# Optimization experiments

Measured on AMD Instinct MI355X. Metric: run time of the kernel, lower is better.

## Reference

```python
import jax, jax.numpy as jnp
import numpy as np

B, L, D_IN, D_MODEL, D_STATE, D_DISCR, KER = 2, 1024, 512, 1024, 16, 64, 4


def setup_inputs() -> dict:
    ks = jax.random.split(jax.random.key(0), 9)
    s = 0.02
    return {
        "seq": jax.random.normal(ks[0], (B, L, D_IN), jnp.float32),
        "W_in": jax.random.normal(ks[1], (2 * D_MODEL, D_IN), jnp.float32) * s,
        "W_out": jax.random.normal(ks[2], (D_IN, D_MODEL), jnp.float32) * s,
        "W_B": jax.random.normal(ks[3], (D_STATE, D_MODEL), jnp.float32) * s,
        "W_C": jax.random.normal(ks[4], (D_STATE, D_MODEL), jnp.float32) * s,
        "W_D1": jax.random.normal(ks[5], (D_DISCR, D_MODEL), jnp.float32) * s,
        "W_D2": jax.random.normal(ks[6], (D_MODEL, D_DISCR), jnp.float32) * s,
        "conv_w": jax.random.normal(ks[7], (D_MODEL, 1, KER), jnp.float32) * 0.1,
        "conv_b": jax.random.normal(ks[8], (D_MODEL,), jnp.float32) * 0.01,
        "A": jnp.tile(jnp.arange(1, D_STATE + 1, dtype=jnp.float32), (D_MODEL, 1)),
        "D": jnp.ones((D_MODEL,), jnp.float32),
    }


def _causal_depthwise_conv(x, w, b):
    # x: [B, L, D] -> torch Conv1d(groups=D, padding=KER-1) truncated to first L outputs
    x = jnp.swapaxes(x, 1, 2)  # [B, D, L]
    y = jax.lax.conv_general_dilated(
        x, w, window_strides=(1,), padding=[(KER - 1, 0)],
        dimension_numbers=("NCH", "OIH", "NCH"), feature_group_count=D_MODEL)
    y = y + b[None, :, None]
    return jnp.swapaxes(y, 1, 2)  # [B, L, D]


def _ssm(x, W_B, W_C, W_D1, W_D2, A, D):
    # x: [B, L, D]
    exp_negA = jnp.exp(-A)                                  # [D, S]
    Bm = jnp.einsum("bld,sd->bls", x, W_B)                  # [B, L, S]
    Cm = jnp.einsum("bld,sd->bls", x, W_C)                  # [B, L, S]
    delta = jax.nn.softplus(D + jnp.einsum("ble,de->bld", jnp.einsum("bld,ed->ble", x, W_D1), W_D2))  # [B, L, D]
    A_bar = exp_negA[None, None] * delta[..., None]         # [B, L, D, S]
    X = Bm[:, :, None, :] * delta[..., None] * x[..., None]  # [B, L, D, S]

    def comb(c1, c2):
        a1, x1 = c1
        a2, x2 = c2
        return a1 * a2, a2 * x1 + x2

    _, h = jax.lax.associative_scan(comb, (A_bar, X), axis=1)  # h: [B, L, D, S]
    y = jnp.einsum("blds,bls->bld", h, Cm)
    return y + D * x


def reference(seq, W_in, W_out, W_B, W_C, W_D1, W_D2, conv_w, conv_b, A, D):
    ab = jnp.einsum("bli,oi->blo", seq, W_in)   # [B, L, 2*D_MODEL]
    a, b = ab[..., :D_MODEL], ab[..., D_MODEL:]
    a = jax.nn.silu(_causal_depthwise_conv(a, conv_w, conv_b))
    a = _ssm(a, W_B, W_C, W_D1, W_D2, A, D)
    out = a * jax.nn.silu(b)
    return jnp.einsum("bld,od->blo", out, W_out)  # [B, L, D_IN]
```

## Files before the change

### kernel.cpp

```cpp
#include <hip/hip_runtime.h>
#include <hip/hip_bf16.h>

using bf16 = __hip_bfloat16;
typedef short short8 __attribute__((ext_vector_type(8)));
typedef float float4v __attribute__((ext_vector_type(4)));

#define B_   2
#define L_   1024
#define DIN  512
#define DM   1024
#define DS   16
#define DD   64
#define KER_ 4
#define NROW (B_*L_)

#define SD   8
#define SC   32
#define SLC  32
#define SDP  9

__device__ __forceinline__ float silu_f(float v){ return v / (1.f + expf(-v)); }

__device__ __forceinline__ short f2bf(float f) {
  union { float f; unsigned u; } v; v.f = f;
  return (short)((v.u + 0x7FFF + ((v.u >> 16) & 1)) >> 16);
}

template<int MW, int NW, int MT, int NT, int EP, int KS, int B3SRC>
__global__ __launch_bounds__(256)
void mfma_nt(const float* __restrict__ A, const float* __restrict__ B,
             const float* __restrict__ B2, const float* __restrict__ B3,
             float* __restrict__ C, const float* __restrict__ Dv,
             int M, int N, int K, int lda, int ldb, int ldc) {
  constexpr int BM = MW * MT * 16;
  constexpr int BN = NW * NT * 16;
  constexpr int TU = (BM + BN) * 4;
  constexpr int NU = (TU + 255) / 256;
  __shared__ short As[BM * 40];
  __shared__ short Bs[BN * 40];
  const int m0 = blockIdx.y * BM;
  const int n0 = blockIdx.x * BN;
  const int tid  = threadIdx.x;
  const int lane = tid & 63;
  const int wave = tid >> 6;
  const int wm   = wave % MW;
  const int wn   = wave / MW;
  const int r16  = lane & 15;
  const int quad = lane >> 4;
  const int kb   = (KS > 1) ? blockIdx.z : 0;
  const int kper = K / KS;
  const int kbeg = kb * kper;
  const int kend = kbeg + kper;

  float4v acc[MT][NT];
#pragma unroll
  for (int i = 0; i < MT; i++)
#pragma unroll
    for (int j = 0; j < NT; j++) acc[i][j] = (float4v){0.f, 0.f, 0.f, 0.f};

  float4 pf0[NU], pf1[NU];
  auto ldu = [&](int j, int k0) {
    int u = tid + j * 256;
    if (u < TU) {
      const float4* p;
      if (u < BM * 4) {
        int row = u >> 2, q = u & 3;
        p = (const float4*)(A + (size_t)(m0 + row) * lda + k0 + q * 8);
      } else {
        int v = u - BM * 4; int row = v >> 2, q = v & 3;
        if (B3SRC) {
          int r = n0 + row;
          const float* bp = (r < 16) ? (B + (size_t)r * ldb)
                          : (r < 32) ? (B2 + (size_t)(r - 16) * ldb)
                                     : (B3 + (size_t)(r - 32) * ldb);
          p = (const float4*)(bp + k0 + q * 8);
        } else {
          p = (const float4*)(B + (size_t)(n0 + row) * ldb + k0 + q * 8);
        }
      }
      pf0[j] = p[0]; pf1[j] = p[1];
    }
  };
  auto stu = [&](int j) {
    int u = tid + j * 256;
    if (u < TU) {
      short8 s = { f2bf(pf0[j].x), f2bf(pf0[j].y), f2bf(pf0[j].z), f2bf(pf0[j].w),
                   f2bf(pf1[j].x), f2bf(pf1[j].y), f2bf(pf1[j].z), f2bf(pf1[j].w) };
      if (u < BM * 4) {
        int row = u >> 2, q = u & 3;
        *(short8*)&As[row * 40 + q * 8] = s;
      } else {
        int v = u - BM * 4; int row = v >> 2, q = v & 3;
        *(short8*)&Bs[row * 40 + q * 8] = s;
      }
    }
  };

#pragma unroll
  for (int j = 0; j < NU; j++) ldu(j, kbeg);

  for (int k0 = kbeg; k0 < kend; k0 += 32) {
#pragma unroll
    for (int j = 0; j < NU; j++) stu(j);
    __syncthreads();
    if (k0 + 32 < kend) {
#pragma unroll
      for (int j = 0; j < NU; j++) ldu(j, k0 + 32);
    }
    short8 afr[MT], bfr[NT];
#pragma unroll
    for (int mi = 0; mi < MT; mi++)
      afr[mi] = *(const short8*)&As[(wm * MT * 16 + mi * 16 + r16) * 40 + quad * 8];
#pragma unroll
    for (int ni = 0; ni < NT; ni++)
      bfr[ni] = *(const short8*)&Bs[(wn * NT * 16 + ni * 16 + r16) * 40 + quad * 8];
#pragma unroll
    for (int mi = 0; mi < MT; mi++)
#pragma unroll
      for (int ni = 0; ni < NT; ni++)
        acc[mi][ni] = __builtin_amdgcn_mfma_f32_16x16x32_bf16(
            afr[mi], bfr[ni], acc[mi][ni], 0, 0, 0);
    __syncthreads();
  }

  float* Cp = C + (size_t)kb * M * ldc;
#pragma unroll
  for (int mi = 0; mi < MT; mi++)
#pragma unroll
    for (int ni = 0; ni < NT; ni++) {
      int gn = n0 + wn * NT * 16 + ni * 16 + r16;
#pragma unroll
      for (int r = 0; r < 4; r++) {
        int gm = m0 + wm * MT * 16 + mi * 16 + quad * 4 + r;
        float v = acc[mi][ni][r];
        if (EP == 1) {
          v += Dv[gn];
          v = fmaxf(v, 0.f) + log1pf(expf(-fabsf(v)));
        }
        Cp[(size_t)gm * ldc + gn] = v;
      }
    }
}

template<int KS>
__global__ __launch_bounds__(256)
void red_k(const float* __restrict__ part, float* __restrict__ dst, int nelem) {
  int i = blockIdx.x * 256 + threadIdx.x;
  float s = 0.f;
#pragma unroll
  for (int j = 0; j < KS; j++) s += part[(size_t)j * nelem + i];
  dst[i] = s;
}

__global__ __launch_bounds__(256)
void conv_silu_k(const float* __restrict__ ab, const float* __restrict__ cw,
                 const float* __restrict__ cb, float* __restrict__ x) {
  int idx = blockIdx.x * 256 + threadIdx.x;
  int d  = idx & (DM - 1);
  int n  = idx >> 10;
  int l  = n & (L_ - 1);
  int bb = n >> 10;
  float acc = cb[d];
#pragma unroll
  for (int k = 0; k < KER_; k++) {
    int ll = l - (KER_ - 1) + k;
    if (ll >= 0) acc += ab[(size_t)(bb * L_ + ll) * (2 * DM) + d] * cw[d * KER_ + k];
  }
  x[idx] = silu_f(acc);
}

__global__ __launch_bounds__(256)
void scan_fused_k(const float* __restrict__ x, const float* __restrict__ dlt,
                  const float* __restrict__ pall, const float* __restrict__ A,
                  const float* __restrict__ Dv, const float* __restrict__ ab,
                  float* __restrict__ sout) {
  __shared__ float Pl[SC][DS][SDP];
  __shared__ float Hl[SC][DS][SDP];
  const int blk = blockIdx.x;
  const int b   = blk >> 7;
  const int d0  = (blk & 127) * SD;
  const int dd  = threadIdx.x & (SD - 1);
  const int c   = threadIdx.x >> 3;
  const int d   = d0 + dd;

  float e[DS];
#pragma unroll
  for (int s = 0; s < DS; s++) e[s] = expf(-A[d * DS + s]);
  const int nbase = b * L_ + c * SLC;

  float h[DS], p[DS];
#pragma unroll
  for (int s = 0; s < DS; s++) { h[s] = 0.f; p[s] = 1.f; }
  for (int i = 0; i < SLC; i++) {
    int n = nbase + i;
    float dl = dlt[(size_t)n * DM + d];
    float xv = x[(size_t)n * DM + d];
    float dx = dl * xv;
    const float4* bm4 = (const float4*)(pall + (size_t)n * 96);
    float4 b0 = bm4[0], b1 = bm4[1], b2 = bm4[2], b3 = bm4[3];
    const float* bm = (const float*)&b0;
    float bmv[DS] = { b0.x,b0.y,b0.z,b0.w, b1.x,b1.y,b1.z,b1.w,
                      b2.x,b2.y,b2.z,b2.w, b3.x,b3.y,b3.z,b3.w };
    (void)bm;
#pragma unroll
    for (int s = 0; s < DS; s++) {
      float a_ = e[s] * dl;
      h[s] = a_ * h[s] + bmv[s] * dx;
      p[s] *= a_;
    }
  }
#pragma unroll
  for (int s = 0; s < DS; s++) { Pl[c][s][dd] = p[s]; Hl[c][s][dd] = h[s]; }
  __syncthreads();

  if (threadIdx.x < DS * SD) {
    int s2  = threadIdx.x >> 3;
    int dd2 = threadIdx.x & (SD - 1);
    float H = 0.f;
    for (int c2 = 0; c2 < SC; c2++) {
      float pp = Pl[c2][s2][dd2];
      float hh = Hl[c2][s2][dd2];
      Pl[c2][s2][dd2] = H;
      H = pp * H + hh;
    }
  }
  __syncthreads();

#pragma unroll
  for (int s = 0; s < DS; s++) h[s] = Pl[c][s][dd];
  float Dd = Dv[d];
  for (int i = 0; i < SLC; i++) {
    int n = nbase + i;
    float dl = dlt[(size_t)n * DM + d];
    float xv = x[(size_t)n * DM + d];
    float dx = dl * xv;
    const float4* bm4 = (const float4*)(pall + (size_t)n * 96);
    float4 b0 = bm4[0], b1 = bm4[1], b2 = bm4[2], b3 = bm4[3];
    float4 c0 = bm4[4], c1 = bm4[5], c2v = bm4[6], c3 = bm4[7];
    float bmv[DS] = { b0.x,b0.y,b0.z,b0.w, b1.x,b1.y,b1.z,b1.w,
                      b2.x,b2.y,b2.z,b2.w, b3.x,b3.y,b3.z,b3.w };
    float cmv[DS] = { c0.x,c0.y,c0.z,c0.w, c1.x,c1.y,c1.z,c1.w,
                      c2v.x,c2v.y,c2v.z,c2v.w, c3.x,c3.y,c3.z,c3.w };
    float y = 0.f;
#pragma unroll
    for (int s = 0; s < DS; s++) {
      h[s] = e[s] * dl * h[s] + bmv[s] * dx;
      y += h[s] * cmv[s];
    }
    y += Dd * xv;
    float g = ab[(size_t)n * (2 * DM) + DM + d];
    sout[(size_t)n * DM + d] = y * silu_f(g);
  }
}

extern "C" void kernel_launch(void* const* d_in, const int* in_sizes, int n_in,
                              void* d_out, int out_size, void* d_ws, size_t ws_size,
                              hipStream_t stream) {
  const float* seq  = (const float*)d_in[0];
  const float* Win  = (const float*)d_in[1];
  const float* Wout = (const float*)d_in[2];
  const float* WB   = (const float*)d_in[3];
  const float* WC   = (const float*)d_in[4];
  const float* WD1  = (const float*)d_in[5];
  const float* WD2  = (const float*)d_in[6];
  const float* cw   = (const float*)d_in[7];
  const float* cb   = (const float*)d_in[8];
  const float* A    = (const float*)d_in[9];
  const float* Dv   = (const float*)d_in[10];
  float* out = (float*)d_out;

  float* ws   = (float*)d_ws;
  float* ab   = ws;
  float* x    = ab   + 4194304;
  float* dlt  = x    + 2097152;
  float* pall = dlt  + 2097152;
  float* t1    = pall + 32;
  float* sout  = x;
  float* ppart = dlt;
  float* gpart = ab;

  mfma_nt<2, 2, 4, 2, 0, 1, 0><<<dim3((2 * DM) / 64, NROW / 128, 1), 256, 0, stream>>>(
      seq, Win, nullptr, nullptr, ab, nullptr, NROW, 2 * DM, DIN, DIN, DIN, 2 * DM);
  conv_silu_k<<<NROW * DM / 256, 256, 0, stream>>>(ab, cw, cb, x);
  mfma_nt<4, 1, 1, 6, 0, 8, 1><<<dim3(1, NROW / 64, 8), 256, 0, stream>>>(
      x, WB, WC, WD1, ppart, nullptr, NROW, 96, DM, DM, DM, 96);
  red_k<8><<<NROW * 96 / 256, 256, 0, stream>>>(ppart, pall, NROW * 96);
  mfma_nt<2, 2, 2, 2, 1, 1, 0><<<dim3(DM / 64, NROW / 64, 1), 256, 0, stream>>>(
      t1, WD2, nullptr, nullptr, dlt, Dv, NROW, DM, DD, 96, DD, DM);
  scan_fused_k<<<B_ * (DM / SD), 256, 0, stream>>>(x, dlt, pall, A, Dv, ab, sout);
  mfma_nt<2, 2, 2, 2, 0, 2, 0><<<dim3(DIN / 64, NROW / 64, 2), 256, 0, stream>>>(
      sout, Wout, nullptr, nullptr, gpart, nullptr, NROW, DIN, DM, DM, DM, DIN);
  red_k<2><<<NROW * DIN / 256, 256, 0, stream>>>(gpart, out, NROW * DIN);
}
```

Baseline: 185.1 us.

## Fuse causal conv+SiLU into projection GEMM and scan; replace split-K reductions with atomics

The standalone conv+SiLU kernel and its materialized x buffer are removed. The projection GEMM now recomputes conv+SiLU from four taps of ab while loading its A tile, and the scan recomputes x with a sliding register window. Both split-K reduction kernels are replaced by atomicAdd epilogues into buffers zeroed with memsets, and bf16 conversion now uses a packed intrinsic. This drops several launches and a full-size intermediate round trip. The cost is redundant tap loads and conv arithmetic in the GEMM loader, plus nondeterministic atomic summation order.

Measured after the change: 180.4 us. -2.5%, faster.

```diff
diff --git a/kernel.cpp b/kernel.cpp
--- a/kernel.cpp
+++ b/kernel.cpp
@@ -21,16 +21,18 @@
 
 __device__ __forceinline__ float silu_f(float v){ return v / (1.f + expf(-v)); }
 
-__device__ __forceinline__ short f2bf(float f) {
-  union { float f; unsigned u; } v; v.f = f;
-  return (short)((v.u + 0x7FFF + ((v.u >> 16) & 1)) >> 16);
+__device__ __forceinline__ short2 f2bf2(float a, float b) {
+  __hip_bfloat162 h = __float22bfloat162_rn(float2{a, b});
+  union { __hip_bfloat162 h; short2 s; } u; u.h = h; return u.s;
 }
 
-template<int MW, int NW, int MT, int NT, int EP, int KS, int B3SRC>
+template<int MW, int NW, int MT, int NT, int EP, int KS, int B3SRC, int CONVA>
 __global__ __launch_bounds__(256)
 void mfma_nt(const float* __restrict__ A, const float* __restrict__ B,
              const float* __restrict__ B2, const float* __restrict__ B3,
              float* __restrict__ C, const float* __restrict__ Dv,
+             const float* __restrict__ abp, const float* __restrict__ cw,
+             const float* __restrict__ cb,
              int M, int N, int K, int lda, int ldb, int ldc) {
   constexpr int BM = MW * MT * 16;
   constexpr int BN = NW * NT * 16;
@@ -61,38 +63,68 @@
   float4 pf0[NU], pf1[NU];
   auto ldu = [&](int j, int k0) {
     int u = tid + j * 256;
-    if (u < TU) {
-      const float4* p;
-      if (u < BM * 4) {
-        int row = u >> 2, q = u & 3;
-        p = (const float4*)(A + (size_t)(m0 + row) * lda + k0 + q * 8);
-      } else {
-        int v = u - BM * 4; int row = v >> 2, q = v & 3;
-        if (B3SRC) {
-          int r = n0 + row;
-          const float* bp = (r < 16) ? (B + (size_t)r * ldb)
-                          : (r < 32) ? (B2 + (size_t)(r - 16) * ldb)
-                                     : (B3 + (size_t)(r - 32) * ldb);
-          p = (const float4*)(bp + k0 + q * 8);
+    if (u >= TU) return;
+    if (CONVA && u < BM * 4) {
+      int row = u >> 2, q = u & 3;
+      int n = m0 + row, l = n & (L_ - 1), bq = n >> 10;
+      float4 tap0[KER_], tap1[KER_];
+#pragma unroll
+      for (int t = 0; t < KER_; t++) {
+        int ll = l - (KER_ - 1) + t;
+        if (ll >= 0) {
+          const float4* p = (const float4*)(abp + (size_t)(bq * L_ + ll) * lda + k0 + q * 8);
+          tap0[t] = p[0]; tap1[t] = p[1];
         } else {
-          p = (const float4*)(B + (size_t)(n0 + row) * ldb + k0 + q * 8);
+          tap0[t] = float4{0.f,0.f,0.f,0.f}; tap1[t] = float4{0.f,0.f,0.f,0.f};
         }
       }
-      pf0[j] = p[0]; pf1[j] = p[1];
-    }
+      float r[8];
+#pragma unroll
+      for (int e = 0; e < 8; e++) {
+        int d = k0 + q * 8 + e;
+        float4 w = *(const float4*)(cw + d * 4);
+        float a = cb[d];
+#pragma unroll
+        for (int t = 0; t < KER_; t++) {
+          float te = (e < 4) ? (&tap0[t].x)[e] : (&tap1[t].x)[e - 4];
+          a += te * (&w.x)[t];
+        }
+        r[e] = silu_f(a);
+      }
+      pf0[j] = float4{r[0], r[1], r[2], r[3]};
+      pf1[j] = float4{r[4], r[5], r[6], r[7]};
+      return;
+    }
+    const float4* p;
+    if (u < BM * 4) {
+      int row = u >> 2, q = u & 3;
+      p = (const float4*)(A + (size_t)(m0 + row) * lda + k0 + q * 8);
+    } else {
+      int v = u - BM * 4; int row = v >> 2, q = v & 3;
+      if (B3SRC) {
+        int rr = n0 + row;
+        const float* bp = (rr < 16) ? (B + (size_t)rr * ldb)
+                        : (rr < 32) ? (B2 + (size_t)(rr - 16) * ldb)
+                                    : (B3 + (size_t)(rr - 32) * ldb);
+        p = (const float4*)(bp + k0 + q * 8);
+      } else {
+        p = (const float4*)(B + (size_t)(n0 + row) * ldb + k0 + q * 8);
+      }
+    }
+    pf0[j] = p[0]; pf1[j] = p[1];
   };
   auto stu = [&](int j) {
     int u = tid + j * 256;
-    if (u < TU) {
-      short8 s = { f2bf(pf0[j].x), f2bf(pf0[j].y), f2bf(pf0[j].z), f2bf(pf0[j].w),
-                   f2bf(pf1[j].x), f2bf(pf1[j].y), f2bf(pf1[j].z), f2bf(pf1[j].w) };
-      if (u < BM * 4) {
-        int row = u >> 2, q = u & 3;
-        *(short8*)&As[row * 40 + q * 8] = s;
-      } else {
-        int v = u - BM * 4; int row = v >> 2, q = v & 3;
-        *(short8*)&Bs[row * 40 + q * 8] = s;
-      }
+    if (u >= TU) return;
+    short2 s0 = f2bf2(pf0[j].x, pf0[j].y), s1 = f2bf2(pf0[j].z, pf0[j].w);
+    short2 s2 = f2bf2(pf1[j].x, pf1[j].y), s3 = f2bf2(pf1[j].z, pf1[j].w);
+    short8 s = { s0.x, s0.y, s1.x, s1.y, s2.x, s2.y, s3.x, s3.y };
+    if (u < BM * 4) {
+      int row = u >> 2, q = u & 3;
+      *(short8*)&As[row * 40 + q * 8] = s;
+    } else {
+      int v = u - BM * 4; int row = v >> 2, q = v & 3;
+      *(short8*)&Bs[row * 40 + q * 8] = s;
     }
   };
 
@@ -123,7 +155,7 @@
     __syncthreads();
   }
 
-  float* Cp = C + (size_t)kb * M * ldc;
+  float* Cp = C + ((EP == 2) ? (size_t)0 : (size_t)kb * M * ldc);
 #pragma unroll
   for (int mi = 0; mi < MT; mi++)
 #pragma unroll
@@ -136,44 +168,21 @@
         if (EP == 1) {
           v += Dv[gn];
           v = fmaxf(v, 0.f) + log1pf(expf(-fabsf(v)));
+          Cp[(size_t)gm * ldc + gn] = v;
+        } else if (EP == 2) {
+          atomicAdd(&Cp[(size_t)gm * ldc + gn], v);
+        } else {
+          Cp[(size_t)gm * ldc + gn] = v;
         }
-        Cp[(size_t)gm * ldc + gn] = v;
       }
     }
 }
 
-template<int KS>
 __global__ __launch_bounds__(256)
-void red_k(const float* __restrict__ part, float* __restrict__ dst, int nelem) {
-  int i = blockIdx.x * 256 + threadIdx.x;
-  float s = 0.f;
-#pragma unroll
-  for (int j = 0; j < KS; j++) s += part[(size_t)j * nelem + i];
-  dst[i] = s;
-}
-
-__global__ __launch_bounds__(256)
-void conv_silu_k(const float* __restrict__ ab, const float* __restrict__ cw,
-                 const float* __restrict__ cb, float* __restrict__ x) {
-  int idx = blockIdx.x * 256 + threadIdx.x;
-  int d  = idx & (DM - 1);
-  int n  = idx >> 10;
-  int l  = n & (L_ - 1);
-  int bb = n >> 10;
-  float acc = cb[d];
-#pragma unroll
-  for (int k = 0; k < KER_; k++) {
-    int ll = l - (KER_ - 1) + k;
-    if (ll >= 0) acc += ab[(size_t)(bb * L_ + ll) * (2 * DM) + d] * cw[d * KER_ + k];
-  }
-  x[idx] = silu_f(acc);
-}
-
-__global__ __launch_bounds__(256)
-void scan_fused_k(const float* __restrict__ x, const float* __restrict__ dlt,
+void scan_fused_k(const float* __restrict__ ab, const float* __restrict__ dlt,
                   const float* __restrict__ pall, const float* __restrict__ A,
-                  const float* __restrict__ Dv, const float* __restrict__ ab,
-                  float* __restrict__ sout) {
+                  const float* __restrict__ Dv, const float* __restrict__ cw,
+                  const float* __restrict__ cb, float* __restrict__ sout) {
   __shared__ float Pl[SC][DS][SDP];
   __shared__ float Hl[SC][DS][SDP];
   const int blk = blockIdx.x;
@@ -186,22 +195,30 @@
   float e[DS];
 #pragma unroll
   for (int s = 0; s < DS; s++) e[s] = expf(-A[d * DS + s]);
-  const int nbase = b * L_ + c * SLC;
-
+  const int   lbase = c * SLC;
+  const int   nbase = b * L_ + lbase;
+  const float4 w    = *(const float4*)(cw + d * 4);
+  const float  cbv  = cb[d];
+
+  auto abA = [&](int l) -> float {
+    return (l >= 0) ? ab[(size_t)(b * L_ + l) * (2 * DM) + d] : 0.f;
+  };
+
+  float r0 = abA(lbase - 3), r1 = abA(lbase - 2), r2 = abA(lbase - 1);
   float h[DS], p[DS];
 #pragma unroll
   for (int s = 0; s < DS; s++) { h[s] = 0.f; p[s] = 1.f; }
   for (int i = 0; i < SLC; i++) {
     int n = nbase + i;
+    float a3 = ab[(size_t)n * (2 * DM) + d];
+    float xv = silu_f(cbv + r0 * w.x + r1 * w.y + r2 * w.z + a3 * w.w);
+    r0 = r1; r1 = r2; r2 = a3;
     float dl = dlt[(size_t)n * DM + d];
-    float xv = x[(size_t)n * DM + d];
     float dx = dl * xv;
     const float4* bm4 = (const float4*)(pall + (size_t)n * 96);
     float4 b0 = bm4[0], b1 = bm4[1], b2 = bm4[2], b3 = bm4[3];
-    const float* bm = (const float*)&b0;
     float bmv[DS] = { b0.x,b0.y,b0.z,b0.w, b1.x,b1.y,b1.z,b1.w,
                       b2.x,b2.y,b2.z,b2.w, b3.x,b3.y,b3.z,b3.w };
-    (void)bm;
 #pragma unroll
     for (int s = 0; s < DS; s++) {
       float a_ = e[s] * dl;
@@ -229,10 +246,13 @@
 #pragma unroll
   for (int s = 0; s < DS; s++) h[s] = Pl[c][s][dd];
   float Dd = Dv[d];
+  r0 = abA(lbase - 3); r1 = abA(lbase - 2); r2 = abA(lbase - 1);
   for (int i = 0; i < SLC; i++) {
     int n = nbase + i;
+    float a3 = ab[(size_t)n * (2 * DM) + d];
+    float xv = silu_f(cbv + r0 * w.x + r1 * w.y + r2 * w.z + a3 * w.w);
+    r0 = r1; r1 = r2; r2 = a3;
     float dl = dlt[(size_t)n * DM + d];
-    float xv = x[(size_t)n * DM + d];
     float dx = dl * xv;
     const float4* bm4 = (const float4*)(pall + (size_t)n * 96);
     float4 b0 = bm4[0], b1 = bm4[1], b2 = bm4[2], b3 = bm4[3];
@@ -271,24 +291,24 @@
 
   float* ws   = (float*)d_ws;
   float* ab   = ws;
-  float* x    = ab   + 4194304;
-  float* dlt  = x    + 2097152;
+  float* dlt  = ab   + 4194304;
   float* pall = dlt  + 2097152;
-  float* t1    = pall + 32;
-  float* sout  = x;
-  float* ppart = dlt;
-  float* gpart = ab;
-
-  mfma_nt<2, 2, 4, 2, 0, 1, 0><<<dim3((2 * DM) / 64, NROW / 128, 1), 256, 0, stream>>>(
-      seq, Win, nullptr, nullptr, ab, nullptr, NROW, 2 * DM, DIN, DIN, DIN, 2 * DM);
-  conv_silu_k<<<NROW * DM / 256, 256, 0, stream>>>(ab, cw, cb, x);
-  mfma_nt<4, 1, 1, 6, 0, 8, 1><<<dim3(1, NROW / 64, 8), 256, 0, stream>>>(
-      x, WB, WC, WD1, ppart, nullptr, NROW, 96, DM, DM, DM, 96);
-  red_k<8><<<NROW * 96 / 256, 256, 0, stream>>>(ppart, pall, NROW * 96);
-  mfma_nt<2, 2, 2, 2, 1, 1, 0><<<dim3(DM / 64, NROW / 64, 1), 256, 0, stream>>>(
-      t1, WD2, nullptr, nullptr, dlt, Dv, NROW, DM, DD, 96, DD, DM);
-  scan_fused_k<<<B_ * (DM / SD), 256, 0, stream>>>(x, dlt, pall, A, Dv, ab, sout);
-  mfma_nt<2, 2, 2, 2, 0, 2, 0><<<dim3(DIN / 64, NROW / 64, 2), 256, 0, stream>>>(
-      sout, Wout, nullptr, nullptr, gpart, nullptr, NROW, DIN, DM, DM, DM, DIN);
-  red_k<2><<<NROW * DIN / 256, 256, 0, stream>>>(gpart, out, NROW * DIN);
+  float* sout = pall + 196608;
+  float* t1   = pall + 32;
+
+  hipMemsetAsync(out, 0, (size_t)NROW * DIN * 4, stream);
+  hipMemsetAsync(pall, 0, (size_t)NROW * 96 * 4, stream);
+  mfma_nt<2, 2, 4, 2, 0, 1, 0, 0><<<dim3((2 * DM) / 64, NROW / 128, 1), 256, 0, stream>>>(
+      seq, Win, nullptr, nullptr, ab, nullptr, nullptr, nullptr, nullptr,
+      NROW, 2 * DM, DIN, DIN, DIN, 2 * DM);
+  mfma_nt<4, 1, 1, 6, 2, 8, 1, 1><<<dim3(1, NROW / 64, 8), 256, 0, stream>>>(
+      nullptr, WB, WC, WD1, pall, nullptr, ab, cw, cb,
+      NROW, 96, DM, 2 * DM, DM, 96);
+  mfma_nt<2, 2, 2, 2, 1, 1, 0, 0><<<dim3(DM / 64, NROW / 64, 1), 256, 0, stream>>>(
+      t1, WD2, nullptr, nullptr, dlt, Dv, nullptr, nullptr, nullptr,
+      NROW, DM, DD, 96, DD, DM);
+  scan_fused_k<<<B_ * (DM / SD), 256, 0, stream>>>(ab, dlt, pall, A, Dv, cw, cb, sout);
+  mfma_nt<2, 2, 2, 2, 2, 2, 0, 0><<<dim3(DIN / 64, NROW / 64, 2), 256, 0, stream>>>(
+      sout, Wout, nullptr, nullptr, out, nullptr, nullptr, nullptr, nullptr,
+      NROW, DIN, DM, DM, DM, DIN);
 }
```
